# Kernel tuning notes

Measured on AMD Instinct MI355X. Metric: run time of the kernel, lower is better.

Reference implementation:

```python
import jax, jax.numpy as jnp
import numpy as np

# Fano plane lines: for each line (i, j, k) we combine colonies i and j and write to k.
FANO_LINES = np.array([(0, 1, 2), (0, 3, 4), (0, 5, 6), (1, 3, 5), (4, 1, 6), (3, 2, 6), (4, 2, 5)], dtype=np.int32)

B, C, Z = 131072, 7, 64  # batch, colonies (fixed 7), z_dim


def setup_inputs() -> dict:
    key = jax.random.key(0)
    k1, k2, k3 = jax.random.split(key, 3)
    colony_states = jax.random.normal(k1, (B, C, Z), dtype=jnp.float32)
    # nn.Linear(2*z_dim, z_dim): weight [Z, 2Z], bias [Z]
    lim = 1.0 / np.sqrt(2 * Z)
    W = jax.random.uniform(k2, (Z, 2 * Z), dtype=jnp.float32, minval=-lim, maxval=lim)
    b = jax.random.uniform(k3, (Z,), dtype=jnp.float32, minval=-lim, maxval=lim)
    gates = jnp.ones((7,), dtype=jnp.float32) / 7.0  # nn.Parameter init
    return {"colony_states": colony_states, "W": W, "b": b, "gates": gates}


def reference(colony_states, W, b, gates):
    I = jnp.asarray(FANO_LINES[:, 0])
    J = jnp.asarray(FANO_LINES[:, 1])
    K = jnpp = jnp.asarray(FANO_LINES[:, 2])
    g = jax.nn.softmax(gates)  # [7]
    # Vectorized gather over all 7 lines at once: [B, 7, 2Z]
    combined = jnp.concatenate([colony_states[:, I], colony_states[:, J]], axis=-1)
    # Shared linear applied to every line: [B, 7, Z]
    delta = jnp.einsum('blf,zf->blz', combined, W) + b
    gated = g[None, :, None] * delta
    # Gated scatter-add into target colonies; K has duplicates, .add accumulates.
    deltas = jnp.zeros_like(colony_states).at[:, K].add(gated)
    return colony_states + deltas
```

## Files before the change

kernel.cpp:

```cpp
#include <hip/hip_runtime.h>
#include <math.h>


using bf16x8  = __attribute__((ext_vector_type(8))) __bf16;
using floatx4 = __attribute__((ext_vector_type(4))) float;

#define TPW 4

__device__ __forceinline__ bf16x8 cvt8(floatx4 a, floatx4 b) {
    bf16x8 r;
    r[0]=(__bf16)a[0]; r[1]=(__bf16)a[1]; r[2]=(__bf16)a[2]; r[3]=(__bf16)a[3];
    r[4]=(__bf16)b[0]; r[5]=(__bf16)b[1]; r[6]=(__bf16)b[2]; r[7]=(__bf16)b[3];
    return r;
}

__global__ __launch_bounds__(256, 2)
void fano_kernel(const float* __restrict__ S,
                 const float* __restrict__ W,
                 const float* __restrict__ bias,
                 const float* __restrict__ gates,
                 float* __restrict__ out, int nt)
{
    __shared__ __align__(16) unsigned char Wb[64 * 256];

    const int tid  = threadIdx.x;
    const int lane = tid & 63;
    const int wave = tid >> 6;
    const int nl   = lane & 15;
    const int qg   = lane >> 4;

    #pragma unroll
    for (int k = 0; k < 4; ++k) {
        const int idx = tid + k * 256;
        const int z = idx >> 4, u = idx & 15;
        const float* src = W + z * 128 + u * 8;
        bf16x8 v = cvt8(*(const floatx4*)src, *(const floatx4*)(src + 4));
        *(bf16x8*)(Wb + z * 256 + ((u ^ (z & 15)) << 4)) = v;
    }

    float g[7];
    {
        float mx = gates[0];
        #pragma unroll
        for (int i = 1; i < 7; ++i) mx = fmaxf(mx, gates[i]);
        float se = 0.f;
        #pragma unroll
        for (int i = 0; i < 7; ++i) { g[i] = __expf(gates[i] - mx); se += g[i]; }
        const float inv = 1.f / se;
        #pragma unroll
        for (int i = 0; i < 7; ++i) g[i] *= inv;
    }

    floatx4 bv[4];
    #pragma unroll
    for (int t = 0; t < 4; ++t) bv[t] = *(const floatx4*)(bias + t * 16 + qg * 4);

    __syncthreads();

    const int wid = blockIdx.x * 4 + wave;

    for (int i = 0; i < TPW; ++i) {
        const int tile = wid * TPW + i;
        if (tile >= nt) break;

        const long long rb = ((long long)tile * 16 + nl) * 448;
        const float* srow = S + rb;
        float*       orow = out + rb;

        floatx4 tmp[6][4];
        #pragma unroll
        for (int c = 0; c < 6; ++c) {
            const float* p = srow + c * 64 + qg * 8;
            tmp[c][0] = *(const floatx4*)p;
            tmp[c][1] = *(const floatx4*)(p + 4);
            tmp[c][2] = *(const floatx4*)(p + 32);
            tmp[c][3] = *(const floatx4*)(p + 36);
        }
        floatx4 cp[3][4];
        #pragma unroll
        for (int j = 0; j < 3; ++j) {
            const int c = (j == 2) ? 3 : j;
            #pragma unroll
            for (int t = 0; t < 4; ++t)
                cp[j][t] = *(const floatx4*)(srow + c * 64 + t * 16 + qg * 4);
        }

        bf16x8 sb[6][2];
        #pragma unroll
        for (int c = 0; c < 6; ++c) {
            sb[c][0] = cvt8(tmp[c][0], tmp[c][1]);
            sb[c][1] = cvt8(tmp[c][2], tmp[c][3]);
        }

        #pragma unroll
        for (int j = 0; j < 3; ++j) {
            const int c = (j == 2) ? 3 : j;
            #pragma unroll
            for (int t = 0; t < 4; ++t)
                *(floatx4*)(orow + c * 64 + t * 16 + qg * 4) = cp[j][t];
        }

        floatx4 res[4][4];
        #pragma unroll
        for (int j = 0; j < 4; ++j) {
            const int c = (j == 0) ? 2 : (j == 1) ? 4 : (j == 2) ? 5 : 6;
            #pragma unroll
            for (int t = 0; t < 4; ++t)
                res[j][t] = *(const floatx4*)(srow + c * 64 + t * 16 + qg * 4);
        }

        #pragma unroll
        for (int hb = 0; hb < 2; ++hb) {
            floatx4 acc[8][2];
            #pragma unroll
            for (int s8 = 0; s8 < 8; ++s8) {
                acc[s8][0] = (floatx4){0.f,0.f,0.f,0.f};
                acc[s8][1] = (floatx4){0.f,0.f,0.f,0.f};
            }
            #pragma unroll
            for (int tp = 0; tp < 2; ++tp) {
                const int t    = hb * 2 + tp;
                const int rowb = (t * 16 + nl) * 256;
                #pragma unroll
                for (int h = 0; h < 4; ++h) {
                    const bf16x8 wf =
                        *(const bf16x8*)(Wb + rowb + (((h * 4 + qg) ^ nl) << 4));
                    const int kb = h & 1;
                    if (h < 2) {
                        acc[0][tp] = __builtin_amdgcn_mfma_f32_16x16x32_bf16(wf, sb[0][kb], acc[0][tp], 0,0,0);
                        acc[1][tp] = __builtin_amdgcn_mfma_f32_16x16x32_bf16(wf, sb[1][kb], acc[1][tp], 0,0,0);
                        acc[2][tp] = __builtin_amdgcn_mfma_f32_16x16x32_bf16(wf, sb[3][kb], acc[2][tp], 0,0,0);
                        acc[3][tp] = __builtin_amdgcn_mfma_f32_16x16x32_bf16(wf, sb[4][kb], acc[3][tp], 0,0,0);
                    } else {
                        acc[4][tp] = __builtin_amdgcn_mfma_f32_16x16x32_bf16(wf, sb[1][kb], acc[4][tp], 0,0,0);
                        acc[5][tp] = __builtin_amdgcn_mfma_f32_16x16x32_bf16(wf, sb[2][kb], acc[5][tp], 0,0,0);
                        acc[6][tp] = __builtin_amdgcn_mfma_f32_16x16x32_bf16(wf, sb[3][kb], acc[6][tp], 0,0,0);
                        acc[7][tp] = __builtin_amdgcn_mfma_f32_16x16x32_bf16(wf, sb[5][kb], acc[7][tp], 0,0,0);
                    }
                }
            }
            #pragma unroll
            for (int tp = 0; tp < 2; ++tp) {
                const int t = hb * 2 + tp;
                const floatx4 b4 = bv[t];
                floatx4 o2 = res[0][t] + g[0] * (acc[0][tp] + acc[4][tp] + b4);
                floatx4 o4 = res[1][t] + g[1] * (acc[0][tp] + acc[6][tp] + b4);
                floatx4 o5 = res[2][t] + g[3] * (acc[1][tp] + acc[6][tp] + b4)
                                       + g[6] * (acc[3][tp] + acc[5][tp] + b4);
                floatx4 o6 = res[3][t] + g[2] * (acc[0][tp] + acc[7][tp] + b4)
                                       + g[4] * (acc[3][tp] + acc[4][tp] + b4)
                                       + g[5] * (acc[2][tp] + acc[5][tp] + b4);
                *(floatx4*)(orow + 2 * 64 + t * 16 + qg * 4) = o2;
                *(floatx4*)(orow + 4 * 64 + t * 16 + qg * 4) = o4;
                *(floatx4*)(orow + 5 * 64 + t * 16 + qg * 4) = o5;
                *(floatx4*)(orow + 6 * 64 + t * 16 + qg * 4) = o6;
            }
        }
    }
}

extern "C" void kernel_launch(void* const* d_in, const int* in_sizes, int n_in,
                              void* d_out, int out_size, void* d_ws, size_t ws_size,
                              hipStream_t stream) {
    const float* S     = (const float*)d_in[0];
    const float* W     = (const float*)d_in[1];
    const float* bias  = (const float*)d_in[2];
    const float* gates = (const float*)d_in[3];
    float* out = (float*)d_out;

    const int B  = in_sizes[0] / (7 * 64);
    const int nt = B / 16;
    const int tiles_per_block = 4 * TPW;
    int grid = (nt + tiles_per_block - 1) / tiles_per_block;
    fano_kernel<<<grid, 256, 0, stream>>>(S, W, bias, gates, out, nt);
}
```

Baseline: 429.8 us.

## Persistent blocks with double-buffered LDS staging of input tiles and register-resident weights

Replaces the per-wave independent tile loop with a persistent grid of 768 blocks. Each block cooperatively stages a 16-row tile of colonies 0-5 into a swizzled, double-buffered LDS buffer and prefetches the next tile into registers while computing the current one. Each wave now owns a 16-column slice of the output features and keeps its W fragments in registers instead of reading them from LDS. Input reads become fully coalesced and are reused from LDS for MFMA operands, residuals and pass-through copies. In exchange it adds a block-wide barrier per tile and more LDS use, and it targets three blocks per CU.

```diff
diff --git a/kernel.cpp b/kernel.cpp
--- a/kernel.cpp
+++ b/kernel.cpp
@@ -4,8 +4,6 @@
 
 using bf16x8  = __attribute__((ext_vector_type(8))) __bf16;
 using floatx4 = __attribute__((ext_vector_type(4))) float;
-
-#define TPW 4
 
 __device__ __forceinline__ bf16x8 cvt8(floatx4 a, floatx4 b) {
     bf16x8 r;
@@ -14,29 +12,23 @@
     return r;
 }
 
-__global__ __launch_bounds__(256, 2)
+#define LDSF(c, row, slot) ((((c) << 8) | ((row) << 4) | (slot)) << 2)
+
+__global__ __launch_bounds__(256, 3)
 void fano_kernel(const float* __restrict__ S,
                  const float* __restrict__ W,
                  const float* __restrict__ bias,
                  const float* __restrict__ gates,
                  float* __restrict__ out, int nt)
 {
-    __shared__ __align__(16) unsigned char Wb[64 * 256];
+    __shared__ float buf[2][6144];
 
     const int tid  = threadIdx.x;
     const int lane = tid & 63;
-    const int wave = tid >> 6;
+    const int w    = tid >> 6;
     const int nl   = lane & 15;
     const int qg   = lane >> 4;
-
-    #pragma unroll
-    for (int k = 0; k < 4; ++k) {
-        const int idx = tid + k * 256;
-        const int z = idx >> 4, u = idx & 15;
-        const float* src = W + z * 128 + u * 8;
-        bf16x8 v = cvt8(*(const floatx4*)src, *(const floatx4*)(src + 4));
-        *(bf16x8*)(Wb + z * 256 + ((u ^ (z & 15)) << 4)) = v;
-    }
+    const int bq   = w * 4 + qg;
 
     float g[7];
     {
@@ -51,111 +43,102 @@
         for (int i = 0; i < 7; ++i) g[i] *= inv;
     }
 
-    floatx4 bv[4];
+    const floatx4 bv = *(const floatx4*)(bias + bq * 4);
+
+    bf16x8 wf[4];
     #pragma unroll
-    for (int t = 0; t < 4; ++t) bv[t] = *(const floatx4*)(bias + t * 16 + qg * 4);
+    for (int h = 0; h < 4; ++h) {
+        const float* p = W + (w * 16 + nl) * 128 + h * 32 + qg * 8;
+        wf[h] = cvt8(*(const floatx4*)p, *(const floatx4*)(p + 4));
+    }
 
+    long long tile = blockIdx.x;
+    if (tile >= nt) return;
+    int cur = 0;
+
+    {
+        const float* sp = S + tile * 7168 + bq * 448;
+        #pragma unroll
+        for (int c = 0; c < 6; ++c) {
+            floatx4 v = *(const floatx4*)(sp + c * 64 + nl * 4);
+            *(floatx4*)(&buf[0][LDSF(c, bq, nl ^ bq)]) = v;
+        }
+    }
     __syncthreads();
 
-    const int wid = blockIdx.x * 4 + wave;
+    for (;;) {
+        const long long next = tile + gridDim.x;
+        const bool more = next < (long long)nt;
+        const long long tb = tile * 7168;
 
-    for (int i = 0; i < TPW; ++i) {
-        const int tile = wid * TPW + i;
-        if (tile >= nt) break;
+        floatx4 stg[6];
+        if (more) {
+            const float* sp = S + next * 7168 + bq * 448;
+            #pragma unroll
+            for (int c = 0; c < 6; ++c)
+                stg[c] = *(const floatx4*)(sp + c * 64 + nl * 4);
+        }
+        const floatx4 res6 = *(const floatx4*)(S + tb + nl * 448 + 384 + bq * 4);
 
-        const long long rb = ((long long)tile * 16 + nl) * 448;
-        const float* srow = S + rb;
-        float*       orow = out + rb;
+        const float* bc = buf[cur];
 
-        floatx4 tmp[6][4];
+        floatx4 acc[8];
         #pragma unroll
-        for (int c = 0; c < 6; ++c) {
-            const float* p = srow + c * 64 + qg * 8;
-            tmp[c][0] = *(const floatx4*)p;
-            tmp[c][1] = *(const floatx4*)(p + 4);
-            tmp[c][2] = *(const floatx4*)(p + 32);
-            tmp[c][3] = *(const floatx4*)(p + 36);
-        }
-        floatx4 cp[3][4];
+        for (int s8 = 0; s8 < 8; ++s8) acc[s8] = (floatx4){0.f, 0.f, 0.f, 0.f};
         #pragma unroll
-        for (int j = 0; j < 3; ++j) {
-            const int c = (j == 2) ? 3 : j;
+        for (int kb = 0; kb < 2; ++kb) {
+            bf16x8 sb[6];
+            const int u0 = kb * 8 + qg * 2;
             #pragma unroll
-            for (int t = 0; t < 4; ++t)
-                cp[j][t] = *(const floatx4*)(srow + c * 64 + t * 16 + qg * 4);
-        }
-
-        bf16x8 sb[6][2];
-        #pragma unroll
-        for (int c = 0; c < 6; ++c) {
-            sb[c][0] = cvt8(tmp[c][0], tmp[c][1]);
-            sb[c][1] = cvt8(tmp[c][2], tmp[c][3]);
+            for (int c = 0; c < 6; ++c) {
+                floatx4 f0 = *(const floatx4*)(bc + LDSF(c, nl, (u0    ) ^ nl));
+                floatx4 f1 = *(const floatx4*)(bc + LDSF(c, nl, (u0 + 1) ^ nl));
+                sb[c] = cvt8(f0, f1);
+            }
+            acc[0] = __builtin_amdgcn_mfma_f32_16x16x32_bf16(wf[kb],     sb[0], acc[0], 0,0,0);
+            acc[1] = __builtin_amdgcn_mfma_f32_16x16x32_bf16(wf[kb],     sb[1], acc[1], 0,0,0);
+            acc[2] = __builtin_amdgcn_mfma_f32_16x16x32_bf16(wf[kb],     sb[3], acc[2], 0,0,0);
+            acc[3] = __builtin_amdgcn_mfma_f32_16x16x32_bf16(wf[kb],     sb[4], acc[3], 0,0,0);
+            acc[4] = __builtin_amdgcn_mfma_f32_16x16x32_bf16(wf[2 + kb], sb[1], acc[4], 0,0,0);
+            acc[5] = __builtin_amdgcn_mfma_f32_16x16x32_bf16(wf[2 + kb], sb[2], acc[5], 0,0,0);
+            acc[6] = __builtin_amdgcn_mfma_f32_16x16x32_bf16(wf[2 + kb], sb[3], acc[6], 0,0,0);
+            acc[7] = __builtin_amdgcn_mfma_f32_16x16x32_bf16(wf[2 + kb], sb[5], acc[7], 0,0,0);
         }
 
         #pragma unroll
         for (int j = 0; j < 3; ++j) {
             const int c = (j == 2) ? 3 : j;
-            #pragma unroll
-            for (int t = 0; t < 4; ++t)
-                *(floatx4*)(orow + c * 64 + t * 16 + qg * 4) = cp[j][t];
+            floatx4 v = *(const floatx4*)(bc + LDSF(c, bq, nl ^ bq));
+            *(floatx4*)(out + tb + bq * 448 + c * 64 + nl * 4) = v;
         }
 
-        floatx4 res[4][4];
-        #pragma unroll
-        for (int j = 0; j < 4; ++j) {
-            const int c = (j == 0) ? 2 : (j == 1) ? 4 : (j == 2) ? 5 : 6;
+        const floatx4 r2 = *(const floatx4*)(bc + LDSF(2, nl, bq ^ nl));
+        const floatx4 r4 = *(const floatx4*)(bc + LDSF(4, nl, bq ^ nl));
+        const floatx4 r5 = *(const floatx4*)(bc + LDSF(5, nl, bq ^ nl));
+
+        floatx4 o2 = r2   + g[0] * (acc[0] + acc[4] + bv);
+        floatx4 o4 = r4   + g[1] * (acc[0] + acc[6] + bv);
+        floatx4 o5 = r5   + g[3] * (acc[1] + acc[6] + bv)
+                          + g[6] * (acc[3] + acc[5] + bv);
+        floatx4 o6 = res6 + g[2] * (acc[0] + acc[7] + bv)
+                          + g[4] * (acc[3] + acc[4] + bv)
+                          + g[5] * (acc[2] + acc[5] + bv);
+        float* op = out + tb + nl * 448 + bq * 4;
+        *(floatx4*)(op + 2 * 64) = o2;
+        *(floatx4*)(op + 4 * 64) = o4;
+        *(floatx4*)(op + 5 * 64) = o5;
+        *(floatx4*)(op + 6 * 64) = o6;
+
+        if (more) {
+            float* bn = buf[cur ^ 1];
             #pragma unroll
-            for (int t = 0; t < 4; ++t)
-                res[j][t] = *(const floatx4*)(srow + c * 64 + t * 16 + qg * 4);
+            for (int c = 0; c < 6; ++c)
+                *(floatx4*)(bn + LDSF(c, bq, nl ^ bq)) = stg[c];
         }
-
-        #pragma unroll
-        for (int hb = 0; hb < 2; ++hb) {
-            floatx4 acc[8][2];
-            #pragma unroll
-            for (int s8 = 0; s8 < 8; ++s8) {
-                acc[s8][0] = (floatx4){0.f,0.f,0.f,0.f};
-                acc[s8][1] = (floatx4){0.f,0.f,0.f,0.f};
-            }
-            #pragma unroll
-            for (int tp = 0; tp < 2; ++tp) {
-                const int t    = hb * 2 + tp;
-                const int rowb = (t * 16 + nl) * 256;
-                #pragma unroll
-                for (int h = 0; h < 4; ++h) {
-                    const bf16x8 wf =
-                        *(const bf16x8*)(Wb + rowb + (((h * 4 + qg) ^ nl) << 4));
-                    const int kb = h & 1;
-                    if (h < 2) {
-                        acc[0][tp] = __builtin_amdgcn_mfma_f32_16x16x32_bf16(wf, sb[0][kb], acc[0][tp], 0,0,0);
-                        acc[1][tp] = __builtin_amdgcn_mfma_f32_16x16x32_bf16(wf, sb[1][kb], acc[1][tp], 0,0,0);
-                        acc[2][tp] = __builtin_amdgcn_mfma_f32_16x16x32_bf16(wf, sb[3][kb], acc[2][tp], 0,0,0);
-                        acc[3][tp] = __builtin_amdgcn_mfma_f32_16x16x32_bf16(wf, sb[4][kb], acc[3][tp], 0,0,0);
-                    } else {
-                        acc[4][tp] = __builtin_amdgcn_mfma_f32_16x16x32_bf16(wf, sb[1][kb], acc[4][tp], 0,0,0);
-                        acc[5][tp] = __builtin_amdgcn_mfma_f32_16x16x32_bf16(wf, sb[2][kb], acc[5][tp], 0,0,0);
-                        acc[6][tp] = __builtin_amdgcn_mfma_f32_16x16x32_bf16(wf, sb[3][kb], acc[6][tp], 0,0,0);
-                        acc[7][tp] = __builtin_amdgcn_mfma_f32_16x16x32_bf16(wf, sb[5][kb], acc[7][tp], 0,0,0);
-                    }
-                }
-            }
-            #pragma unroll
-            for (int tp = 0; tp < 2; ++tp) {
-                const int t = hb * 2 + tp;
-                const floatx4 b4 = bv[t];
-                floatx4 o2 = res[0][t] + g[0] * (acc[0][tp] + acc[4][tp] + b4);
-                floatx4 o4 = res[1][t] + g[1] * (acc[0][tp] + acc[6][tp] + b4);
-                floatx4 o5 = res[2][t] + g[3] * (acc[1][tp] + acc[6][tp] + b4)
-                                       + g[6] * (acc[3][tp] + acc[5][tp] + b4);
-                floatx4 o6 = res[3][t] + g[2] * (acc[0][tp] + acc[7][tp] + b4)
-                                       + g[4] * (acc[3][tp] + acc[4][tp] + b4)
-                                       + g[5] * (acc[2][tp] + acc[5][tp] + b4);
-                *(floatx4*)(orow + 2 * 64 + t * 16 + qg * 4) = o2;
-                *(floatx4*)(orow + 4 * 64 + t * 16 + qg * 4) = o4;
-                *(floatx4*)(orow + 5 * 64 + t * 16 + qg * 4) = o5;
-                *(floatx4*)(orow + 6 * 64 + t * 16 + qg * 4) = o6;
-            }
-        }
+        __syncthreads();
+        if (!more) break;
+        tile = next;
+        cur ^= 1;
     }
 }
 
@@ -170,7 +153,7 @@
 
     const int B  = in_sizes[0] / (7 * 64);
     const int nt = B / 16;
-    const int tiles_per_block = 4 * TPW;
-    int grid = (nt + tiles_per_block - 1) / tiles_per_block;
+    int grid = 768;
+    if (grid > nt) grid = nt;
     fano_kernel<<<grid, 256, 0, stream>>>(S, W, bias, gates, out, nt);
 }
```

Result: faster. 397.7 us (-7.5%).
